# Kernel optimization log

Measured on AMD Instinct MI355X. Metric: run time of the kernel, lower is better.

The kernel has to match this reference:

```python
import jax, jax.numpy as jnp
import numpy as np

BETA = 0.25
K = 1024   # num_codebook_vectors
D = 256    # latent_dim


def setup_inputs() -> dict:
    key = jax.random.key(0)
    k1, k2 = jax.random.split(key)
    z = jax.random.normal(k1, (32, D, 32, 32), dtype=jnp.float32)
    # original init: uniform(-1/K, 1/K)
    codebook = jax.random.uniform(k2, (K, D), dtype=jnp.float32, minval=-1.0 / K, maxval=1.0 / K)
    return {"z": z, "codebook": codebook}


def reference(z, codebook):
    B, C, H, W = z.shape
    sg = jax.lax.stop_gradient
    # NCHW -> NHWC, flatten to [N, D]
    z_nhwc = jnp.transpose(z, (0, 2, 3, 1))
    zf = z_nhwc.reshape(-1, C)
    # squared distances via sum-of-squares + matmul: [N, K]
    d = (jnp.sum(zf * zf, axis=1, keepdims=True)
         + jnp.sum(codebook * codebook, axis=1)
         - 2.0 * jnp.matmul(zf, codebook.T))
    idx = jnp.argmin(d, axis=1)                      # [N]
    z_q = codebook[idx].reshape(B, H, W, C)          # gather + reshape
    # commitment + codebook loss
    loss = (jnp.mean((sg(z_q) - z_nhwc) ** 2)
            + BETA * jnp.mean((z_q - sg(z_nhwc)) ** 2))
    # straight-through estimator
    z_q = z_nhwc + sg(z_q - z_nhwc)
    z_q = jnp.transpose(z_q, (0, 3, 1, 2))           # back to NCHW
    return z_q, idx, loss
```

## Files before the change

kernel.cpp:

```cpp
#include <hip/hip_runtime.h>

constexpr int D_ = 256;
constexpr int K_ = 1024;
constexpr int P_ = 1024;
constexpr int N_ = 32768;

constexpr int IDX_OFF  = 8388608;
constexpr int LOSS_OFF = 8421376;

constexpr int CB16_OFF = 0;
constexpr int CN_OFF   = 262400;
constexpr int ZN_OFF   = 263424;
constexpr int CNT_OFF  = 296448;
constexpr int WL_OFF   = 296449;

constexpr float RESCUE_MARGIN = 1e-4f;

typedef _Float16 half8 __attribute__((ext_vector_type(8)));
typedef float f32x4 __attribute__((ext_vector_type(4)));

__device__ __forceinline__ void stage16(const float* g, float* l) {
  __builtin_amdgcn_global_load_lds(
      (const __attribute__((address_space(1))) unsigned int*)g,
      (__attribute__((address_space(3))) unsigned int*)l, 16, 0, 0);
}

__global__ __launch_bounds__(64) void vq_prep(const float* __restrict__ z,
                                              const float* __restrict__ cb,
                                              float* __restrict__ scratch,
                                              float* __restrict__ loss) {
  const int blk = blockIdx.x;
  const int lane = threadIdx.x;
  if (blk < 512) {
    const int n0 = blk * 64;
    const int b = n0 >> 10, p0 = n0 & (P_ - 1);
    const float* zp = z + (size_t)b * (D_ * P_) + p0 + lane;
    float a8[8];
    #pragma unroll
    for (int i = 0; i < 8; ++i) a8[i] = 0.0f;
    for (int oct = 0; oct < 32; ++oct) {
      #pragma unroll
      for (int i = 0; i < 8; ++i) {
        float v = zp[(size_t)(oct * 8 + i) * P_];
        a8[i] = fmaf(v, v, a8[i]);
      }
    }
    scratch[ZN_OFF + n0 + lane] = ((a8[0] + a8[1]) + (a8[2] + a8[3])) +
                                  ((a8[4] + a8[5]) + (a8[6] + a8[7]));
    if (blk == 0 && lane == 0) {
      *loss = 0.0f;
      ((int*)(scratch + CNT_OFF))[0] = 0;
    }
  } else if (blk < 1536) {
    const int k = blk - 512;
    const float* row = cb + (size_t)k * D_;
    double s = 0.0;
    #pragma unroll
    for (int i = 0; i < 4; ++i) {
      double v = (double)row[lane + i * 64];
      s = fma(v, v, s);
    }
    #pragma unroll
    for (int off = 32; off; off >>= 1) s += __shfl_down(s, off, 64);
    if (lane == 0) scratch[CN_OFF + k] = (float)s;
  } else {
    const int kt = blk - 1536;
    const int k = kt * 16 + (lane & 15);
    const int quad = lane >> 4;
    _Float16* cw = (_Float16*)(scratch + CB16_OFF);
    for (int ds = 0; ds < 8; ++ds) {
      const float* src = cb + (size_t)k * D_ + ds * 32 + quad * 8;
      half8 h, lo;
      #pragma unroll
      for (int j = 0; j < 8; ++j) {
        const float v = src[j] * 1024.0f;
        const _Float16 hh = (_Float16)v;
        h[j] = hh;
        lo[j] = (_Float16)(v - (float)hh);
      }
      const int s = kt * 8 + ds;
      *(half8*)(cw + ((size_t)(s * 2 + 0) * 64 + lane) * 8) = h;
      *(half8*)(cw + ((size_t)(s * 2 + 1) * 64 + lane) * 8) = lo;
    }
  }
}

__global__ __launch_bounds__(256, 2) void vq_mfma(const float* __restrict__ z,
                                                  float* __restrict__ scratch,
                                                  float* __restrict__ idxf) {
  const int t = threadIdx.x;
  const int w = t >> 6;
  const int l = t & 63;
  const int quad = l >> 4;
  const int col = l & 15;
  const int rh = w & 1;
  const int cs = w >> 1;
  const int n0 = blockIdx.x * 64;
  const int b = n0 >> 10;
  const int p0 = n0 & (P_ - 1);

  const float* __restrict__ cbsw_f = scratch + CB16_OFF;
  const float* __restrict__ cnorm = scratch + CN_OFF;
  const float* __restrict__ zn = scratch + ZN_OFF;

  __shared__ alignas(16) float Bbuf[2][2][4096];
  __shared__ alignas(16) float cnLds[1024];
  __shared__ float sM1[4][32];
  __shared__ float sM2[4][32];
  __shared__ int   sI1[4][32];
  float* Azs = &Bbuf[0][1][0];

  *(float4*)(cnLds + t * 4) = *(const float4*)(cnorm + t * 4);

  float znr[2][4];
  #pragma unroll
  for (int rt = 0; rt < 2; ++rt) {
    const float4 znv = *(const float4*)(zn + n0 + rh * 32 + rt * 16 + quad * 4);
    znr[rt][0] = znv.x; znr[rt][1] = znv.y;
    znr[rt][2] = znv.z; znr[rt][3] = znv.w;
  }

  half8 Ah[2][8], Al[2][8];
  const int dl0 = w * 8;
  for (int ds = 0; ds < 8; ++ds) {
    __syncthreads();
    #pragma unroll
    for (int i = 0; i < 8; ++i) {
      const int dloc = dl0 + i;
      Azs[l * 33 + dloc] =
          z[(size_t)b * (D_ * P_) + (size_t)(ds * 32 + dloc) * P_ + p0 + l];
    }
    __syncthreads();
    #pragma unroll
    for (int rt = 0; rt < 2; ++rt) {
      const float* src = &Azs[(rh * 32 + rt * 16 + col) * 33 + quad * 8];
      half8 h, lo;
      #pragma unroll
      for (int j = 0; j < 8; ++j) {
        const float v = src[j];
        const _Float16 hh = (_Float16)v;
        h[j] = hh;
        lo[j] = (_Float16)(v - (float)hh);
      }
      Ah[rt][ds] = h;
      Al[rt][ds] = lo;
    }
  }

  asm volatile("s_waitcnt vmcnt(0)" ::: "memory");

  const int ch0 = rh * 8;
  const float* gsbase = cbsw_f + (size_t)cs * 32 * 4096 + l * 4;
  #pragma unroll
  for (int j = 0; j < 8; ++j) {
    const int chunk = ch0 + j;
    stage16(gsbase + chunk * 256, &Bbuf[cs][0][chunk * 256]);
  }

  float m1[2][4], m2v[2][4];
  int i1[2][4];
  #pragma unroll
  for (int rt = 0; rt < 2; ++rt)
    #pragma unroll
    for (int r = 0; r < 4; ++r) { m1[rt][r] = 1e30f; m2v[rt][r] = 1e30f; i1[rt][r] = 0; }

  float* bcur = &Bbuf[cs][0][0];
  float* bnxt = &Bbuf[cs][1][0];
  const float* cnp = cnLds + cs * 512 + col;
  int kg = cs * 512 + col;

  for (int p = 0; p < 32; ++p) {
    asm volatile("s_waitcnt vmcnt(0)" ::: "memory");
    __builtin_amdgcn_s_barrier();
    __builtin_amdgcn_sched_barrier(0);

    if (p < 31) {
      const float* gsp = gsbase + (size_t)(p + 1) * 4096;
      #pragma unroll
      for (int j = 0; j < 8; ++j) {
        const int chunk = ch0 + j;
        stage16(gsp + chunk * 256, bnxt + chunk * 256);
      }
    }

    const float cnf = *cnp;

    f32x4 aH0 = {0.f,0.f,0.f,0.f}, aM0 = {0.f,0.f,0.f,0.f}, aL0 = {0.f,0.f,0.f,0.f};
    f32x4 aH1 = {0.f,0.f,0.f,0.f}, aM1 = {0.f,0.f,0.f,0.f}, aL1 = {0.f,0.f,0.f,0.f};

    __builtin_amdgcn_s_setprio(1);
    #pragma unroll
    for (int ds = 0; ds < 8; ++ds) {
      const half8 bh = *(const half8*)(bcur + (ds * 2 + 0) * 256 + l * 4);
      const half8 bl = *(const half8*)(bcur + (ds * 2 + 1) * 256 + l * 4);
      aH0 = __builtin_amdgcn_mfma_f32_16x16x32_f16(Ah[0][ds], bh, aH0, 0, 0, 0);
      aH1 = __builtin_amdgcn_mfma_f32_16x16x32_f16(Ah[1][ds], bh, aH1, 0, 0, 0);
      aM0 = __builtin_amdgcn_mfma_f32_16x16x32_f16(Ah[0][ds], bl, aM0, 0, 0, 0);
      aM1 = __builtin_amdgcn_mfma_f32_16x16x32_f16(Ah[1][ds], bl, aM1, 0, 0, 0);
      aL0 = __builtin_amdgcn_mfma_f32_16x16x32_f16(Al[0][ds], bh, aL0, 0, 0, 0);
      aL1 = __builtin_amdgcn_mfma_f32_16x16x32_f16(Al[1][ds], bh, aL1, 0, 0, 0);
    }
    __builtin_amdgcn_s_setprio(0);

    #pragma unroll
    for (int r = 0; r < 4; ++r) {
      const float s0 = fmaf((aH0[r] + aM0[r]) + aL0[r], -0x1p-9f, znr[0][r] + cnf);
      if (s0 < m1[0][r]) { m2v[0][r] = m1[0][r]; m1[0][r] = s0; i1[0][r] = kg; }
      else if (s0 < m2v[0][r]) m2v[0][r] = s0;
      const float s1 = fmaf((aH1[r] + aM1[r]) + aL1[r], -0x1p-9f, znr[1][r] + cnf);
      if (s1 < m1[1][r]) { m2v[1][r] = m1[1][r]; m1[1][r] = s1; i1[1][r] = kg; }
      else if (s1 < m2v[1][r]) m2v[1][r] = s1;
    }

    cnp += 16;
    kg += 16;
    float* tmp = bcur; bcur = bnxt; bnxt = tmp;
  }

  #pragma unroll
  for (int off = 1; off <= 8; off <<= 1) {
    #pragma unroll
    for (int rt = 0; rt < 2; ++rt)
      #pragma unroll
      for (int r = 0; r < 4; ++r) {
        const float o1 = __shfl_xor(m1[rt][r], off, 64);
        const float o2 = __shfl_xor(m2v[rt][r], off, 64);
        const int oi = __shfl_xor(i1[rt][r], off, 64);
        if (o1 < m1[rt][r]) { m2v[rt][r] = fminf(m1[rt][r], o2); m1[rt][r] = o1; i1[rt][r] = oi; }
        else if (o1 == m1[rt][r]) { i1[rt][r] = min(i1[rt][r], oi); m2v[rt][r] = m1[rt][r]; }
        else { m2v[rt][r] = fminf(m2v[rt][r], o1); }
      }
  }

  if (col == 0) {
    #pragma unroll
    for (int rt = 0; rt < 2; ++rt)
      #pragma unroll
      for (int r = 0; r < 4; ++r) {
        const int rl = rt * 16 + quad * 4 + r;
        sM1[w][rl] = m1[rt][r];
        sM2[w][rl] = m2v[rt][r];
        sI1[w][rl] = i1[rt][r];
      }
  }
  __syncthreads();
  if (w < 2 && col == 0) {
    int* cnt = (int*)(scratch + CNT_OFF);
    int* wl = (int*)(scratch + WL_OFF);
    #pragma unroll
    for (int rt = 0; rt < 2; ++rt)
      #pragma unroll
      for (int r = 0; r < 4; ++r) {
        const int rl = rt * 16 + quad * 4 + r;
        float a1 = sM1[w][rl], a2 = sM2[w][rl];
        int ai = sI1[w][rl];
        const float o1 = sM1[w + 2][rl], o2 = sM2[w + 2][rl];
        const int oi = sI1[w + 2][rl];
        if (o1 < a1) { a2 = fminf(a1, o2); a1 = o1; ai = oi; }
        else if (o1 == a1) { ai = min(ai, oi); a2 = a1; }
        else { a2 = fminf(a2, o1); }
        const int n = n0 + w * 32 + rl;
        idxf[n] = (float)ai;
        if (a2 - a1 < RESCUE_MARGIN) {
          const int pos = atomicAdd(cnt, 1);
          wl[pos] = n;
        }
      }
  }
}

__global__ __launch_bounds__(256, 4) void vq_rescue(const float* __restrict__ z,
                                                    const float* __restrict__ cb,
                                                    const float* __restrict__ scratch,
                                                    float* __restrict__ idxf) {
  const int tid = threadIdx.x;
  const float* cnorm = scratch + CN_OFF;
  const float* zn = scratch + ZN_OFF;
  const int count = ((const int*)(scratch + CNT_OFF))[0];
  const int* wl = (const int*)(scratch + WL_OFF);

  __shared__ alignas(16) float zb[8][D_];
  __shared__ int nrow[8];
  __shared__ float rv[256];
  __shared__ int ri[256];

  for (int base = blockIdx.x * 8; base < count; base += gridDim.x * 8) {
    const int take = min(8, count - base);
    if (tid < 8) nrow[tid] = wl[base + (tid < take ? tid : 0)];
    __syncthreads();
    #pragma unroll
    for (int r = 0; r < 8; ++r) {
      const int n = nrow[r];
      const int b = n >> 10, p = n & (P_ - 1);
      zb[r][tid] = z[(size_t)b * (D_ * P_) + (size_t)tid * P_ + p];
    }
    __syncthreads();

    const int k0 = tid * 4;
    const float4* __restrict__ cr0 = (const float4*)(cb + (size_t)(k0 + 0) * D_);
    const float4* __restrict__ cr1 = (const float4*)(cb + (size_t)(k0 + 1) * D_);
    const float4* __restrict__ cr2 = (const float4*)(cb + (size_t)(k0 + 2) * D_);
    const float4* __restrict__ cr3 = (const float4*)(cb + (size_t)(k0 + 3) * D_);

    float acc[8][4];
    #pragma unroll
    for (int r = 0; r < 8; ++r)
      #pragma unroll
      for (int j = 0; j < 4; ++j) acc[r][j] = 0.0f;

    for (int d4 = 0; d4 < 64; ++d4) {
      const float4 v0 = cr0[d4], v1 = cr1[d4], v2 = cr2[d4], v3 = cr3[d4];
      #pragma unroll
      for (int r = 0; r < 8; ++r) {
        const float4 zv = ((const float4*)zb[r])[d4];
        acc[r][0] = fmaf(zv.x, v0.x, acc[r][0]);
        acc[r][0] = fmaf(zv.y, v0.y, acc[r][0]);
        acc[r][0] = fmaf(zv.z, v0.z, acc[r][0]);
        acc[r][0] = fmaf(zv.w, v0.w, acc[r][0]);
        acc[r][1] = fmaf(zv.x, v1.x, acc[r][1]);
        acc[r][1] = fmaf(zv.y, v1.y, acc[r][1]);
        acc[r][1] = fmaf(zv.z, v1.z, acc[r][1]);
        acc[r][1] = fmaf(zv.w, v1.w, acc[r][1]);
        acc[r][2] = fmaf(zv.x, v2.x, acc[r][2]);
        acc[r][2] = fmaf(zv.y, v2.y, acc[r][2]);
        acc[r][2] = fmaf(zv.z, v2.z, acc[r][2]);
        acc[r][2] = fmaf(zv.w, v2.w, acc[r][2]);
        acc[r][3] = fmaf(zv.x, v3.x, acc[r][3]);
        acc[r][3] = fmaf(zv.y, v3.y, acc[r][3]);
        acc[r][3] = fmaf(zv.z, v3.z, acc[r][3]);
        acc[r][3] = fmaf(zv.w, v3.w, acc[r][3]);
      }
    }

    for (int r = 0; r < 8; ++r) {
      const int n = nrow[r];
      const float zA = zn[n];
      float bv = 1e30f;
      int bi = 0x7fffffff;
      #pragma unroll
      for (int j = 0; j < 4; ++j) {
        const float A = zA + cnorm[k0 + j];
        const float s = A - 2.0f * acc[r][j];
        if (s < bv) { bv = s; bi = k0 + j; }
      }
      rv[tid] = bv; ri[tid] = bi;
      __syncthreads();
      for (int off = 128; off >= 1; off >>= 1) {
        if (tid < off) {
          const float ov = rv[tid + off];
          const int oi = ri[tid + off];
          if (ov < rv[tid] || (ov == rv[tid] && oi < ri[tid])) { rv[tid] = ov; ri[tid] = oi; }
        }
        __syncthreads();
      }
      if (tid == 0 && r < take) idxf[n] = (float)ri[0];
      __syncthreads();
    }
  }
}

__global__ __launch_bounds__(256) void vq_gather(const float* __restrict__ z,
                                                 const float* __restrict__ cb,
                                                 const float* __restrict__ idxf,
                                                 float* __restrict__ out,
                                                 float* __restrict__ loss) {
  const int tid = threadIdx.x;
  const int lane = tid & 63;
  const int w = tid >> 6;
  const int n0 = blockIdx.x * 64;
  const int b = n0 >> 10;
  const int p0 = n0 & (P_ - 1);
  const int p = p0 + lane;

  const int idx = (int)(idxf[n0 + lane] + 0.5f);
  const float4* crow4 = (const float4*)(cb + (size_t)idx * D_);
  const size_t base = (size_t)b * (D_ * P_) + p;

  float acc = 0.0f;
  #pragma unroll 4
  for (int ci = 0; ci < 16; ++ci) {
    const float4 v = crow4[w * 16 + ci];
    const int c = w * 64 + ci * 4;
    const float vv[4] = {v.x, v.y, v.z, v.w};
    #pragma unroll
    for (int u = 0; u < 4; ++u) {
      const size_t a = base + (size_t)(c + u) * P_;
      const float zv = z[a];
      const float d = vv[u] - zv;
      out[a] = zv + d;
      acc = fmaf(d, d, acc);
    }
  }
  #pragma unroll
  for (int off = 32; off; off >>= 1) acc += __shfl_down(acc, off, 64);
  __shared__ float wsum[4];
  if (lane == 0) wsum[w] = acc;
  __syncthreads();
  if (tid == 0) {
    float s = wsum[0] + wsum[1] + wsum[2] + wsum[3];
    atomicAdd(loss, s * (1.25f / 8388608.0f));
  }
}

extern "C" void kernel_launch(void* const* d_in, const int* in_sizes, int n_in,
                              void* d_out, int out_size, void* d_ws, size_t ws_size,
                              hipStream_t stream) {
  const float* z = (const float*)d_in[0];
  const float* cb = (const float*)d_in[1];
  float* out = (float*)d_out;

  vq_prep<<<1600, 64, 0, stream>>>(z, cb, out, out + LOSS_OFF);
  vq_mfma<<<N_ / 64, 256, 0, stream>>>(z, out, out + IDX_OFF);
  vq_rescue<<<128, 256, 0, stream>>>(z, cb, out, out + IDX_OFF);
  vq_gather<<<N_ / 64, 256, 0, stream>>>(z, cb, out + IDX_OFF, out, out + LOSS_OFF);
}
```

Measured before the change: 226.7 us.

## Double-buffer MFMA accumulators to overlap argmin with next tile's matmul

Splits the main loop into a matmul phase and an argmin phase, using two sets of accumulators so the argmin comparison for one codebook tile runs after the MFMAs of the following tile are issued. This hides MFMA result latency behind independent work instead of stalling on the accumulators right away. It also doubles the rescue kernel grid from 128 to 256 blocks. The extra accumulator set raises register pressure, which could lower occupancy.

New measurement: 234.0 us. +3.2%, slower.

```diff
diff --git a/kernel.cpp b/kernel.cpp
--- a/kernel.cpp
+++ b/kernel.cpp
@@ -169,7 +169,14 @@
   const float* cnp = cnLds + cs * 512 + col;
   int kg = cs * 512 + col;
 
-  for (int p = 0; p < 32; ++p) {
+  f32x4 AH0, AM0, AL0, AH1, AM1, AL1;
+  f32x4 BH0, BM0, BL0, BH1, BM1, BL1;
+  float cnfA = 0.f, cnfB = 0.f;
+  int kgA = 0, kgB = 0;
+
+  auto do_phase = [&](f32x4& H0, f32x4& M0, f32x4& L0,
+                      f32x4& H1, f32x4& M1, f32x4& L1,
+                      int p, float& cnf_sav, int& kg_sav) {
     asm volatile("s_waitcnt vmcnt(0)" ::: "memory");
     __builtin_amdgcn_s_barrier();
     __builtin_amdgcn_sched_barrier(0);
@@ -183,39 +190,55 @@
       }
     }
 
-    const float cnf = *cnp;
-
-    f32x4 aH0 = {0.f,0.f,0.f,0.f}, aM0 = {0.f,0.f,0.f,0.f}, aL0 = {0.f,0.f,0.f,0.f};
-    f32x4 aH1 = {0.f,0.f,0.f,0.f}, aM1 = {0.f,0.f,0.f,0.f}, aL1 = {0.f,0.f,0.f,0.f};
+    cnf_sav = *cnp;
+    kg_sav = kg;
+
+    H0 = {0.f,0.f,0.f,0.f}; M0 = {0.f,0.f,0.f,0.f}; L0 = {0.f,0.f,0.f,0.f};
+    H1 = {0.f,0.f,0.f,0.f}; M1 = {0.f,0.f,0.f,0.f}; L1 = {0.f,0.f,0.f,0.f};
 
     __builtin_amdgcn_s_setprio(1);
     #pragma unroll
     for (int ds = 0; ds < 8; ++ds) {
       const half8 bh = *(const half8*)(bcur + (ds * 2 + 0) * 256 + l * 4);
       const half8 bl = *(const half8*)(bcur + (ds * 2 + 1) * 256 + l * 4);
-      aH0 = __builtin_amdgcn_mfma_f32_16x16x32_f16(Ah[0][ds], bh, aH0, 0, 0, 0);
-      aH1 = __builtin_amdgcn_mfma_f32_16x16x32_f16(Ah[1][ds], bh, aH1, 0, 0, 0);
-      aM0 = __builtin_amdgcn_mfma_f32_16x16x32_f16(Ah[0][ds], bl, aM0, 0, 0, 0);
-      aM1 = __builtin_amdgcn_mfma_f32_16x16x32_f16(Ah[1][ds], bl, aM1, 0, 0, 0);
-      aL0 = __builtin_amdgcn_mfma_f32_16x16x32_f16(Al[0][ds], bh, aL0, 0, 0, 0);
-      aL1 = __builtin_amdgcn_mfma_f32_16x16x32_f16(Al[1][ds], bh, aL1, 0, 0, 0);
+      H0 = __builtin_amdgcn_mfma_f32_16x16x32_f16(Ah[0][ds], bh, H0, 0, 0, 0);
+      H1 = __builtin_amdgcn_mfma_f32_16x16x32_f16(Ah[1][ds], bh, H1, 0, 0, 0);
+      M0 = __builtin_amdgcn_mfma_f32_16x16x32_f16(Ah[0][ds], bl, M0, 0, 0, 0);
+      M1 = __builtin_amdgcn_mfma_f32_16x16x32_f16(Ah[1][ds], bl, M1, 0, 0, 0);
+      L0 = __builtin_amdgcn_mfma_f32_16x16x32_f16(Al[0][ds], bh, L0, 0, 0, 0);
+      L1 = __builtin_amdgcn_mfma_f32_16x16x32_f16(Al[1][ds], bh, L1, 0, 0, 0);
     }
     __builtin_amdgcn_s_setprio(0);
-
-    #pragma unroll
-    for (int r = 0; r < 4; ++r) {
-      const float s0 = fmaf((aH0[r] + aM0[r]) + aL0[r], -0x1p-9f, znr[0][r] + cnf);
-      if (s0 < m1[0][r]) { m2v[0][r] = m1[0][r]; m1[0][r] = s0; i1[0][r] = kg; }
-      else if (s0 < m2v[0][r]) m2v[0][r] = s0;
-      const float s1 = fmaf((aH1[r] + aM1[r]) + aL1[r], -0x1p-9f, znr[1][r] + cnf);
-      if (s1 < m1[1][r]) { m2v[1][r] = m1[1][r]; m1[1][r] = s1; i1[1][r] = kg; }
-      else if (s1 < m2v[1][r]) m2v[1][r] = s1;
-    }
 
     cnp += 16;
     kg += 16;
     float* tmp = bcur; bcur = bnxt; bnxt = tmp;
-  }
+  };
+
+  auto do_argmin = [&](const f32x4& H0, const f32x4& M0, const f32x4& L0,
+                       const f32x4& H1, const f32x4& M1, const f32x4& L1,
+                       float cnf, int kgp) {
+    #pragma unroll
+    for (int r = 0; r < 4; ++r) {
+      const float s0 = fmaf((H0[r] + M0[r]) + L0[r], -0x1p-9f, znr[0][r] + cnf);
+      if (s0 < m1[0][r]) { m2v[0][r] = m1[0][r]; m1[0][r] = s0; i1[0][r] = kgp; }
+      else if (s0 < m2v[0][r]) m2v[0][r] = s0;
+      const float s1 = fmaf((H1[r] + M1[r]) + L1[r], -0x1p-9f, znr[1][r] + cnf);
+      if (s1 < m1[1][r]) { m2v[1][r] = m1[1][r]; m1[1][r] = s1; i1[1][r] = kgp; }
+      else if (s1 < m2v[1][r]) m2v[1][r] = s1;
+    }
+  };
+
+  do_phase(AH0, AM0, AL0, AH1, AM1, AL1, 0, cnfA, kgA);
+  for (int i = 0; i < 15; ++i) {
+    do_phase(BH0, BM0, BL0, BH1, BM1, BL1, 2 * i + 1, cnfB, kgB);
+    do_argmin(AH0, AM0, AL0, AH1, AM1, AL1, cnfA, kgA);
+    do_phase(AH0, AM0, AL0, AH1, AM1, AL1, 2 * i + 2, cnfA, kgA);
+    do_argmin(BH0, BM0, BL0, BH1, BM1, BL1, cnfB, kgB);
+  }
+  do_phase(BH0, BM0, BL0, BH1, BM1, BL1, 31, cnfB, kgB);
+  do_argmin(AH0, AM0, AL0, AH1, AM1, AL1, cnfA, kgA);
+  do_argmin(BH0, BM0, BL0, BH1, BM1, BL1, cnfB, kgB);
 
   #pragma unroll
   for (int off = 1; off <= 8; off <<= 1) {
@@ -411,6 +434,6 @@
 
   vq_prep<<<1600, 64, 0, stream>>>(z, cb, out, out + LOSS_OFF);
   vq_mfma<<<N_ / 64, 256, 0, stream>>>(z, out, out + IDX_OFF);
-  vq_rescue<<<128, 256, 0, stream>>>(z, cb, out, out + IDX_OFF);
+  vq_rescue<<<256, 256, 0, stream>>>(z, cb, out, out + IDX_OFF);
   vq_gather<<<N_ / 64, 256, 0, stream>>>(z, cb, out + IDX_OFF, out, out + LOSS_OFF);
 }
```
